# Optimization experiments

Measured on AMD Instinct MI355X. Metric: run time of the kernel, lower is better.

## Reference

```python
import jax, jax.numpy as jnp
import numpy as np

EPS = 1e-7
MAX_NORM = 1.0 - 1e-5  # Poincare-ball norm clip (standard in Poincare impls to keep atanh finite)


def _cart_to_sph(p):
    # p: [..., 3] -> (radius, polar theta, azimuth phi)
    x, y, z = p[..., 0], p[..., 1], p[..., 2]
    r = jnp.linalg.norm(p, axis=-1)
    theta = jnp.arccos(jnp.clip(z / jnp.maximum(r, EPS), -1.0, 1.0))
    phi = jnp.arctan2(y, x)
    return jnp.stack((r, theta, phi), axis=-1)


def _sph_to_cart(s):
    r, theta, phi = s[..., 0], s[..., 1], s[..., 2]
    tmp = r * jnp.sin(theta)
    return jnp.stack((tmp * jnp.cos(phi), tmp * jnp.sin(phi), r * jnp.cos(theta)), axis=-1)


def _log0(x):
    # Poincare log map at the origin, c=1: atanh(||x||) * x/||x|| (norm clipped)
    n = jnp.linalg.norm(x, axis=-1, keepdims=True)
    return jnp.arctanh(jnp.minimum(n, MAX_NORM)) * x / jnp.maximum(n, EPS)


def _exp0(v):
    # Poincare exp map at the origin, c=1: tanh(||v||) * v/||v||
    n = jnp.linalg.norm(v, axis=-1, keepdims=True)
    return jnp.tanh(n) * v / jnp.maximum(n, EPS)


def setup_inputs() -> dict:
    key = jax.random.key(0)
    k1, k2 = jax.random.split(key)
    B, H, N, K, M = 256, 2, 1024, 64, 3
    dgms = jax.random.uniform(k1, (B, H, N, 2), dtype=jnp.float32)          # persistence points in [0,1)
    theta = jax.random.uniform(k2, (H, K, M), dtype=jnp.float32,
                               minval=-0.05, maxval=0.05)                    # tf.random_uniform_initializer default
    return {"dgms": dgms, "theta": theta}


def reference(dgms, theta):
    # dgms: [B, H, N, 2], theta: [H, K, 3]
    B, H, N, _ = dgms.shape
    K = theta.shape[1]
    y3 = jnp.pad(dgms, ((0, 0), (0, 0), (0, 0), (0, 1)))                     # pad point to 3D: [B,H,N,3]
    # broadcast-add each basis vector theta[h,k]: [B,H,K,N,3]
    shifted = y3[:, :, None, :, :] + theta[None, :, :, None, :]
    sph = _cart_to_sph(shifted)                                              # [B,H,K,N,3]
    tangent = _log0(sph)                                                     # log map to tangent space at origin
    sums = jnp.sum(tangent, axis=3)                                          # sum over points: [B,H,K,3]
    x_dgm = _exp0(sums)                                                      # back to the manifold
    y_dgm = _sph_to_cart(x_dgm)                                              # [B,H,K,3]
    return y_dgm.reshape(B, H * K * 3)                                       # hom0 block then hom1 block, matching tf concat
```

## Files before the change

kernel.cpp:

```cpp
#include <hip/hip_runtime.h>
#include <hip/hip_bf16.h>

#define B_DIM 256
#define H_DIM 2
#define N_DIM 1024
#define K_DIM 64

#define PI_F      3.14159265358979f
#define HALF_PI_F 1.57079632679490f
#define PI2_4_F   2.46740110027234f
#define MAX_NORM  0.99999f
#define ATANH_MN  6.1030247f
#define RC2       0.0625f

template <int CTRL>
static __device__ __forceinline__ float dpp_f(float x) {
    return __int_as_float(__builtin_amdgcn_update_dpp(
        0, __float_as_int(x), CTRL, 0xF, 0xF, false));
}
static __device__ __forceinline__ float row16_sum(float x) {
    x += dpp_f<0xB1>(x);
    x += dpp_f<0x4E>(x);
    x += dpp_f<0x124>(x);
    x += dpp_f<0x128>(x);
    return x;
}

static __device__ __forceinline__ float atan_poly(float t) {
    float u = t * t;
    float p = fmaf(u, 0.0208351f, -0.0851330f);
    p = fmaf(u, p, 0.1801410f);
    p = fmaf(u, p, -0.3302995f);
    p = fmaf(u, p, 0.9998660f);
    return t * p;
}
static __device__ __forceinline__ float asin_poly(float u) {
    float u2 = u * u;
    float qa = fmaf(u2, 0.0340000f, 0.0303819f);
    qa = fmaf(u2, qa, 0.0446429f);
    qa = fmaf(u2, qa, 0.0750000f);
    qa = fmaf(u2, qa, 0.1666667f);
    return fmaf(u * u2, qa, u);
}
static __device__ __forceinline__ float slow_s(float n2, float ninv) {
    float n = n2 * ninv;
    float m = fminf(n, MAX_NORM);
    float at = 0.34657359f *
               __builtin_amdgcn_logf((1.0f + m) * __builtin_amdgcn_rcpf(1.0f - m));
    return at * ninv;
}
static __device__ __forceinline__ float sin_poly(float u) {
    float u2 = u * u;
    float p = fmaf(u2, -1.9841270e-4f, 8.3333333e-3f);
    p = fmaf(u2, p, -1.6666667e-1f);
    return u * fmaf(u2, p, 1.0f);
}
static __device__ __forceinline__ float cos_poly(float u) {
    float u2 = u * u;
    float p = fmaf(u2, 2.4801587e-5f, -1.3888889e-3f);
    p = fmaf(u2, p, 4.1666667e-2f);
    p = fmaf(u2, p, -0.5f);
    return fmaf(u2, p, 1.0f);
}

static __device__ __forceinline__ void ad_point(float x, float y, float* acc) {
    float q  = fmaf(x, x, y * y);
    float si = __builtin_amdgcn_rsqf(q);
    float u2 = si * si, u3 = si * u2, u4 = u2 * u2;
    float rho = q * si;

    float mn = fminf(x, y);
    float A  = asin_poly(mn * si);
    float phi0 = (y > x) ? (HALF_PI_F - A) : A;

    float phx  = -y * u2, phy = x * u2;
    float phxx = 2.0f * x * y * u4;
    float phxy = (y * y - x * x) * u4;
    float phyy = -phxx;

    float m0  = fmaf(phi0, phi0, q + PI2_4_F);
    float mx  = fmaf(2.0f * phi0, phx, 2.0f * x);
    float my  = fmaf(2.0f * phi0, phy, 2.0f * y);
    float mz  = -PI_F * si;
    float mxx = fmaf(2.0f, fmaf(phx, phx, phi0 * phxx), 2.0f);
    float mxy = 2.0f * fmaf(phx, phy, phi0 * phxy);
    float myy = fmaf(2.0f, fmaf(phy, phy, phi0 * phyy), 2.0f);
    float mzz = fmaf(2.0f, u2, 2.0f);
    float mxz = PI_F * x * u3;
    float myz = PI_F * y * u3;

    float w  = __builtin_amdgcn_rsqf(m0);
    float w2 = w * w, w3 = w * w2;
    float s0 = ATANH_MN * w;
    float A1 = -0.5f * ATANH_MN * w3;
    float A2 = -1.5f * A1 * w2;
    float sx = A1 * mx, sy = A1 * my, sz = A1 * mz;
    float sxx = fmaf(A2 * mx, mx, A1 * mxx);
    float sxy = fmaf(A2 * mx, my, A1 * mxy);
    float syy = fmaf(A2 * my, my, A1 * myy);
    float sxz = fmaf(A2 * mx, mz, A1 * mxz);
    float syz = fmaf(A2 * my, mz, A1 * myz);
    float szz = fmaf(A2 * mz, mz, A1 * mzz);

    float rx = x * si, ry = y * si;
    float rxx = y * y * u3, rxy = -x * y * u3, ryy = x * x * u3;

    acc[0] += s0 * rho;
    acc[1] += fmaf(sx, rho, s0 * rx);
    acc[2] += fmaf(sy, rho, s0 * ry);
    acc[3] += sz * rho;
    acc[4] += fmaf(sxx, rho, fmaf(2.0f * sx, rx, s0 * rxx));
    acc[5] += fmaf(sxy, rho, fmaf(sx, ry, fmaf(sy, rx, s0 * rxy)));
    acc[6] += fmaf(syy, rho, fmaf(2.0f * sy, ry, s0 * ryy));
    acc[7] += fmaf(sxz, rho, sz * rx);
    acc[8] += fmaf(syz, rho, sz * ry);
    acc[9] += fmaf(szz, rho, s0 * si);
    acc[10] += s0 * HALF_PI_F;
    acc[11] += sx * HALF_PI_F;
    acc[12] += sy * HALF_PI_F;
    acc[13] += fmaf(sz, HALF_PI_F, -s0 * si);
    acc[14] += sxx * HALF_PI_F;
    acc[15] += sxy * HALF_PI_F;
    acc[16] += syy * HALF_PI_F;
    acc[17] += fmaf(sxz, HALF_PI_F, fmaf(-sx, si, s0 * x * u3));
    acc[18] += fmaf(syz, HALF_PI_F, fmaf(-sy, si, s0 * y * u3));
    acc[19] += fmaf(szz, HALF_PI_F, -2.0f * sz * si);
    acc[20] += s0 * phi0;
    acc[21] += fmaf(sx, phi0, s0 * phx);
    acc[22] += fmaf(sy, phi0, s0 * phy);
    acc[23] += sz * phi0;
    acc[24] += fmaf(sxx, phi0, fmaf(2.0f * sx, phx, s0 * phxx));
    acc[25] += fmaf(sxy, phi0, fmaf(sx, phy, fmaf(sy, phx, s0 * phxy)));
    acc[26] += fmaf(syy, phi0, fmaf(2.0f * sy, phy, s0 * phyy));
    acc[27] += fmaf(sxz, phi0, sz * phx);
    acc[28] += fmaf(syz, phi0, sz * phy);
    acc[29] += szz * phi0;
}

__global__ __launch_bounds__(256) void pman_fused(const void* __restrict__ dgms,
                                                  const void* __restrict__ theta,
                                                  void* __restrict__ out) {
    __shared__ float  lds_coef[32];
    __shared__ float  lds_part[16][32];
    __shared__ int    lds_cnt;
    __shared__ float2 lds_near[512];

    const int tid  = threadIdx.x;
    const int lane = tid & 63;
    const int wv   = tid >> 6;
    const int bh   = blockIdx.x;
    const int h    = bh & 1;
    if (tid == 0) lds_cnt = 0;
    __syncthreads();

    const unsigned int wrd = ((const unsigned int*)dgms)[lane];
    const bool f32 = __popcll(__ballot((wrd >> 15) & 1u)) > 8;

    const int k   = tid >> 2;
    const int sub = tid & 3;
    float tx, ty, tz;
    {
        const int tb = (h * K_DIM + k) * 3;
        if (f32) {
            const float* t = (const float*)theta;
            tx = t[tb]; ty = t[tb + 1]; tz = t[tb + 2];
        } else {
            const unsigned short* t = (const unsigned short*)theta;
            tx = __uint_as_float(((unsigned int)t[tb]) << 16);
            ty = __uint_as_float(((unsigned int)t[tb + 1]) << 16);
            tz = __uint_as_float(((unsigned int)t[tb + 2]) << 16);
        }
    }

    float px[4], py[4];
    if (f32) {
        const float4* fp = (const float4*)dgms + (bh << 9) + (tid << 1);
        const float4 a = fp[0], b = fp[1];
        px[0] = a.x; py[0] = a.y; px[1] = a.z; py[1] = a.w;
        px[2] = b.x; py[2] = b.y; px[3] = b.z; py[3] = b.w;
    } else {
        const uint4 d = ((const uint4*)dgms)[(bh << 8) + tid];
        px[0] = __uint_as_float(d.x << 16); py[0] = __uint_as_float(d.x & 0xFFFF0000u);
        px[1] = __uint_as_float(d.y << 16); py[1] = __uint_as_float(d.y & 0xFFFF0000u);
        px[2] = __uint_as_float(d.z << 16); py[2] = __uint_as_float(d.z & 0xFFFF0000u);
        px[3] = __uint_as_float(d.w << 16); py[3] = __uint_as_float(d.w & 0xFFFF0000u);
    }

    float acc[30];
    #pragma unroll
    for (int i = 0; i < 30; ++i) acc[i] = 0.0f;

    const unsigned long long lt_mask = (1ull << lane) - 1ull;
    #pragma unroll
    for (int i = 0; i < 4; ++i) {
        float x0 = px[i], y0 = py[i];
        float q = fmaf(x0, x0, y0 * y0);
        const bool isnear = q < RC2;
        unsigned long long nm = __ballot(isnear);
        int base = 0;
        if (lane == 0 && nm) base = atomicAdd(&lds_cnt, __popcll(nm));
        base = __shfl(base, 0);
        if (isnear) {
            lds_near[base + __popcll(nm & lt_mask)] = make_float2(x0, y0);
        } else {
            ad_point(x0, y0, acc);
        }
    }

    #pragma unroll
    for (int i = 0; i < 30; ++i) acc[i] = row16_sum(acc[i]);
    if ((lane & 15) == 0) {
        const int row = (wv << 2) | (lane >> 4);
        #pragma unroll
        for (int i = 0; i < 30; ++i) lds_part[row][i] = acc[i];
    }
    __syncthreads();
    if (tid < 30) {
        float s = 0.0f;
        #pragma unroll
        for (int r = 0; r < 16; ++r) s += lds_part[r][tid];
        lds_coef[tid] = s;
    }
    __syncthreads();

    const float az = fabsf(tz);
    const float ntz = -tz;
    const float inv_tz = __builtin_amdgcn_rcpf((tz == 0.0f) ? 1e-30f : tz);
    const float kbase = (tz < 0.0f) ? PI_F : 0.0f;
    const float z2 = tz * tz;
    const float z2h = 0.5f * z2;
    const float haz_inv = 0.5f * __builtin_amdgcn_rcpf(fmaxf(az, 1e-30f));

    const int cnt = lds_cnt;
    float ar = 0.f, at_ = 0.f, ap = 0.f;
    for (int i = sub; i < cnt; i += 4) {
        float2 pt = lds_near[i];
        float x = pt.x + tx, y = pt.y + ty;
        float rxy2 = fmaf(x, x, fmaf(y, y, 1e-30f));
        float sxyinv = __builtin_amdgcn_rsqf(rxy2);
        float sxy = rxy2 * sxyinv;
        float r2 = rxy2 + z2;
        const bool big = sxy >= az;
        float rr = big ? fmaf(z2h, sxyinv, sxy) : fmaf(haz_inv, rxy2, az);
        float te = big ? ntz * sxyinv : sxy * inv_tz;
        float K  = big ? HALF_PI_F : kbase;
        float th = K + atan_poly(te);
        float ax = fabsf(x), ay = fabsf(y);
        float lo = fminf(ax, ay);
        float u = lo * sxyinv;
        float As = asin_poly(u);
        float p = (ay > ax) ? (HALF_PI_F - As) : As;
        p = (x < 0.0f) ? (PI_F - p) : p;
        p = __uint_as_float(__float_as_uint(p) ^
                            (__float_as_uint(y) & 0x80000000u));
        float n2 = fmaf(th, th, fmaf(p, p, r2));
        float ninv = __builtin_amdgcn_rsqf(n2);
        float s = ATANH_MN * ninv;
        if (__builtin_expect(n2 < 1.0f, 0))
            s = slow_s(n2, ninv);
        ar = fmaf(s, rr, ar);
        at_ = fmaf(s, th, at_);
        ap = fmaf(s, p, ap);
    }
    #pragma unroll
    for (int m = 2; m; m >>= 1) {
        ar += __shfl_xor(ar, m);
        at_ += __shfl_xor(at_, m);
        ap += __shfl_xor(ap, m);
    }

    if (sub == 0) {
        float tx2h = 0.5f * tx * tx, ty2h = 0.5f * ty * ty, tz2h = 0.5f * tz * tz;
        float txty = tx * ty, txtz = tx * tz, tytz = ty * tz;
        float S[3];
        #pragma unroll
        for (int o = 0; o < 3; ++o) {
            const float* cc = lds_coef + o * 10;
            float v = cc[0];
            v = fmaf(cc[1], tx, v);   v = fmaf(cc[2], ty, v);   v = fmaf(cc[3], tz, v);
            v = fmaf(cc[4], tx2h, v); v = fmaf(cc[5], txty, v); v = fmaf(cc[6], ty2h, v);
            v = fmaf(cc[7], txtz, v); v = fmaf(cc[8], tytz, v); v = fmaf(cc[9], tz2h, v);
            S[o] = v;
        }
        float sr = S[0] + ar, st = S[1] + at_, sp = S[2] + ap;
        float n2 = fmaf(sr, sr, fmaf(st, st, sp * sp));
        float rsqn = __builtin_amdgcn_rsqf(fmaxf(n2, 1e-30f));
        float nv = n2 * rsqn;
        float scale = rsqn;
        if (__builtin_expect(nv < 16.0f, 0))
            scale = tanhf(nv) / fmaxf(nv, 1e-7f);
        float rr = scale * sr;
        float th = scale * st;
        float ph = scale * sp;
        float tmp = rr * sin_poly(th);
        const int o = (bh * K_DIM + k) * 3;
        if (f32) {
            float* op = (float*)out;
            op[o]     = tmp * cos_poly(ph);
            op[o + 1] = tmp * sin_poly(ph);
            op[o + 2] = rr * cos_poly(th);
        } else {
            __hip_bfloat16* op = (__hip_bfloat16*)out;
            op[o]     = __float2bfloat16(tmp * cos_poly(ph));
            op[o + 1] = __float2bfloat16(tmp * sin_poly(ph));
            op[o + 2] = __float2bfloat16(rr * cos_poly(th));
        }
    }
}

extern "C" void kernel_launch(void* const* d_in, const int* in_sizes, int n_in,
                              void* d_out, int out_size, void* d_ws, size_t ws_size,
                              hipStream_t stream) {
    (void)in_sizes; (void)n_in; (void)out_size; (void)d_ws; (void)ws_size;
    pman_fused<<<B_DIM * H_DIM, 256, 0, stream>>>(d_in[0], d_in[1], d_out);
}
```

Measured before the change: 64.38 us.

## Split fused kernel into two phases via workspace for more parallelism

Replaces the single fused kernel (one block per batch-head) with a memset plus two kernels. Phase 1 spreads the far-point Taylor-coefficient accumulation and near-point compaction across four blocks per batch-head, using global atomics into a workspace. Phase 2 computes the exact near-point terms with 16 lanes per basis vector and more blocks in total. The aim is more blocks in flight and a shorter serial near-point loop per wave. The cost is extra launches, global atomics and a workspace round-trip. The fused kernel stays as a fallback when the workspace is too small.

```diff
diff --git a/kernel.cpp b/kernel.cpp
--- a/kernel.cpp
+++ b/kernel.cpp
@@ -12,6 +12,12 @@
 #define MAX_NORM  0.99999f
 #define ATANH_MN  6.1030247f
 #define RC2       0.0625f
+
+#define WS_COEF   0
+#define WS_CNT    65536
+#define WS_ZERO_BYTES 67584
+#define WS_NEAR   67584
+#define WS_NEEDED (WS_NEAR + 512 * 1024 * 8)
 
 template <int CTRL>
 static __device__ __forceinline__ float dpp_f(float x) {
@@ -137,6 +143,194 @@
     acc[29] += szz * phi0;
 }
 
+static __device__ __forceinline__ void epilogue(const float* cc30, float ar, float at_,
+                                                float ap, float tx, float ty, float tz,
+                                                int o, bool f32, void* out) {
+    float tx2h = 0.5f * tx * tx, ty2h = 0.5f * ty * ty, tz2h = 0.5f * tz * tz;
+    float txty = tx * ty, txtz = tx * tz, tytz = ty * tz;
+    float S[3];
+    #pragma unroll
+    for (int oo = 0; oo < 3; ++oo) {
+        const float* cc = cc30 + oo * 10;
+        float v = cc[0];
+        v = fmaf(cc[1], tx, v);   v = fmaf(cc[2], ty, v);   v = fmaf(cc[3], tz, v);
+        v = fmaf(cc[4], tx2h, v); v = fmaf(cc[5], txty, v); v = fmaf(cc[6], ty2h, v);
+        v = fmaf(cc[7], txtz, v); v = fmaf(cc[8], tytz, v); v = fmaf(cc[9], tz2h, v);
+        S[oo] = v;
+    }
+    float sr = S[0] + ar, st = S[1] + at_, sp = S[2] + ap;
+    float n2 = fmaf(sr, sr, fmaf(st, st, sp * sp));
+    float rsqn = __builtin_amdgcn_rsqf(fmaxf(n2, 1e-30f));
+    float nv = n2 * rsqn;
+    float scale = rsqn;
+    if (__builtin_expect(nv < 16.0f, 0))
+        scale = tanhf(nv) / fmaxf(nv, 1e-7f);
+    float rr = scale * sr;
+    float th = scale * st;
+    float ph = scale * sp;
+    float tmp = rr * sin_poly(th);
+    if (f32) {
+        float* op = (float*)out;
+        op[o]     = tmp * cos_poly(ph);
+        op[o + 1] = tmp * sin_poly(ph);
+        op[o + 2] = rr * cos_poly(th);
+    } else {
+        __hip_bfloat16* op = (__hip_bfloat16*)out;
+        op[o]     = __float2bfloat16(tmp * cos_poly(ph));
+        op[o + 1] = __float2bfloat16(tmp * sin_poly(ph));
+        op[o + 2] = __float2bfloat16(rr * cos_poly(th));
+    }
+}
+
+static __device__ __forceinline__ void near_term(float x, float y, float tz, float az,
+                                                 float ntz, float inv_tz, float kbase,
+                                                 float z2, float z2h, float haz_inv,
+                                                 float& ar, float& at_, float& ap) {
+    float rxy2 = fmaf(x, x, fmaf(y, y, 1e-30f));
+    float sxyinv = __builtin_amdgcn_rsqf(rxy2);
+    float sxy = rxy2 * sxyinv;
+    float r2 = rxy2 + z2;
+    const bool big = sxy >= az;
+    float rr = big ? fmaf(z2h, sxyinv, sxy) : fmaf(haz_inv, rxy2, az);
+    float te = big ? ntz * sxyinv : sxy * inv_tz;
+    float K  = big ? HALF_PI_F : kbase;
+    float th = K + atan_poly(te);
+    float ax = fabsf(x), ay = fabsf(y);
+    float lo = fminf(ax, ay);
+    float u = lo * sxyinv;
+    float As = asin_poly(u);
+    float p = (ay > ax) ? (HALF_PI_F - As) : As;
+    p = (x < 0.0f) ? (PI_F - p) : p;
+    p = __uint_as_float(__float_as_uint(p) ^ (__float_as_uint(y) & 0x80000000u));
+    float n2 = fmaf(th, th, fmaf(p, p, r2));
+    float ninv = __builtin_amdgcn_rsqf(n2);
+    float s = ATANH_MN * ninv;
+    if (__builtin_expect(n2 < 1.0f, 0))
+        s = slow_s(n2, ninv);
+    ar = fmaf(s, rr, ar);
+    at_ = fmaf(s, th, at_);
+    ap = fmaf(s, p, ap);
+}
+
+__global__ __launch_bounds__(256) void pman_phase1(const void* __restrict__ dgms,
+                                                   void* __restrict__ ws) {
+    __shared__ float lds_part[16][32];
+    const int tid  = threadIdx.x;
+    const int lane = tid & 63;
+    const int wv   = tid >> 6;
+    const int blk  = blockIdx.x;
+    const int bh   = blk >> 2;
+    const int quarter = blk & 3;
+
+    const unsigned int wrd = ((const unsigned int*)dgms)[lane];
+    const bool f32 = __popcll(__ballot((wrd >> 15) & 1u)) > 8;
+
+    const int pt = (bh << 10) + (quarter << 8) + tid;
+    float x0, y0;
+    if (f32) {
+        const float2 d = ((const float2*)dgms)[pt];
+        x0 = d.x; y0 = d.y;
+    } else {
+        const unsigned int d = ((const unsigned int*)dgms)[pt];
+        x0 = __uint_as_float(d << 16);
+        y0 = __uint_as_float(d & 0xFFFF0000u);
+    }
+
+    float*  coef  = (float*)((char*)ws + WS_COEF) + (bh << 5);
+    int*    cnt   = (int*)((char*)ws + WS_CNT);
+    float2* nearp = (float2*)((char*)ws + WS_NEAR) + (bh << 10);
+
+    float acc[30];
+    #pragma unroll
+    for (int i = 0; i < 30; ++i) acc[i] = 0.0f;
+
+    float q = fmaf(x0, x0, y0 * y0);
+    const bool isnear = q < RC2;
+    unsigned long long nm = __ballot(isnear);
+    int base = 0;
+    if (lane == 0 && nm) base = atomicAdd(&cnt[bh], __popcll(nm));
+    base = __shfl(base, 0);
+    if (isnear) {
+        nearp[base + __popcll(nm & ((1ull << lane) - 1ull))] = make_float2(x0, y0);
+    } else {
+        ad_point(x0, y0, acc);
+    }
+
+    #pragma unroll
+    for (int i = 0; i < 30; ++i) acc[i] = row16_sum(acc[i]);
+    if ((lane & 15) == 0) {
+        const int row = (wv << 2) | (lane >> 4);
+        #pragma unroll
+        for (int i = 0; i < 30; ++i) lds_part[row][i] = acc[i];
+    }
+    __syncthreads();
+    if (tid < 30) {
+        float s = 0.0f;
+        #pragma unroll
+        for (int r = 0; r < 16; ++r) s += lds_part[r][tid];
+        atomicAdd(&coef[tid], s);
+    }
+}
+
+__global__ __launch_bounds__(256) void pman_phase2(const void* __restrict__ dgms,
+                                                   const void* __restrict__ theta,
+                                                   void* __restrict__ out,
+                                                   const void* __restrict__ ws) {
+    const int tid  = threadIdx.x;
+    const int lane = tid & 63;
+    const unsigned int wrd = ((const unsigned int*)dgms)[lane];
+    const bool f32 = __popcll(__ballot((wrd >> 15) & 1u)) > 8;
+
+    const int w   = blockIdx.x * 4 + (tid >> 6);
+    const int bh  = w >> 4;
+    const int grp = lane >> 4;
+    const int sub = lane & 15;
+    const int k   = ((w & 15) << 2) + grp;
+    const int h   = bh & 1;
+
+    float tx, ty, tz;
+    {
+        const int tb = (h * K_DIM + k) * 3;
+        if (f32) {
+            const float* t = (const float*)theta;
+            tx = t[tb]; ty = t[tb + 1]; tz = t[tb + 2];
+        } else {
+            const unsigned short* t = (const unsigned short*)theta;
+            tx = __uint_as_float(((unsigned int)t[tb]) << 16);
+            ty = __uint_as_float(((unsigned int)t[tb + 1]) << 16);
+            tz = __uint_as_float(((unsigned int)t[tb + 2]) << 16);
+        }
+    }
+    const float az = fabsf(tz);
+    const float ntz = -tz;
+    const float inv_tz = __builtin_amdgcn_rcpf((tz == 0.0f) ? 1e-30f : tz);
+    const float kbase = (tz < 0.0f) ? PI_F : 0.0f;
+    const float z2 = tz * tz;
+    const float z2h = 0.5f * z2;
+    const float haz_inv = 0.5f * __builtin_amdgcn_rcpf(fmaxf(az, 1e-30f));
+
+    const int cnt = ((const int*)((const char*)ws + WS_CNT))[bh];
+    const float2* np = (const float2*)((const char*)ws + WS_NEAR) + (bh << 10);
+
+    float ar = 0.f, at_ = 0.f, ap = 0.f;
+    for (int i = sub; i < cnt; i += 16) {
+        float2 pt = np[i];
+        near_term(pt.x + tx, pt.y + ty, tz, az, ntz, inv_tz, kbase,
+                  z2, z2h, haz_inv, ar, at_, ap);
+    }
+    ar  = row16_sum(ar);
+    at_ = row16_sum(at_);
+    ap  = row16_sum(ap);
+
+    if (sub == 0) {
+        const float* cc = (const float*)((const char*)ws + WS_COEF) + (bh << 5);
+        float c30[30];
+        #pragma unroll
+        for (int i = 0; i < 30; ++i) c30[i] = cc[i];
+        epilogue(c30, ar, at_, ap, tx, ty, tz, (bh * K_DIM + k) * 3, f32, out);
+    }
+}
+
 __global__ __launch_bounds__(256) void pman_fused(const void* __restrict__ dgms,
                                                   const void* __restrict__ theta,
                                                   void* __restrict__ out) {
@@ -235,32 +429,8 @@
     float ar = 0.f, at_ = 0.f, ap = 0.f;
     for (int i = sub; i < cnt; i += 4) {
         float2 pt = lds_near[i];
-        float x = pt.x + tx, y = pt.y + ty;
-        float rxy2 = fmaf(x, x, fmaf(y, y, 1e-30f));
-        float sxyinv = __builtin_amdgcn_rsqf(rxy2);
-        float sxy = rxy2 * sxyinv;
-        float r2 = rxy2 + z2;
-        const bool big = sxy >= az;
-        float rr = big ? fmaf(z2h, sxyinv, sxy) : fmaf(haz_inv, rxy2, az);
-        float te = big ? ntz * sxyinv : sxy * inv_tz;
-        float K  = big ? HALF_PI_F : kbase;
-        float th = K + atan_poly(te);
-        float ax = fabsf(x), ay = fabsf(y);
-        float lo = fminf(ax, ay);
-        float u = lo * sxyinv;
-        float As = asin_poly(u);
-        float p = (ay > ax) ? (HALF_PI_F - As) : As;
-        p = (x < 0.0f) ? (PI_F - p) : p;
-        p = __uint_as_float(__float_as_uint(p) ^
-                            (__float_as_uint(y) & 0x80000000u));
-        float n2 = fmaf(th, th, fmaf(p, p, r2));
-        float ninv = __builtin_amdgcn_rsqf(n2);
-        float s = ATANH_MN * ninv;
-        if (__builtin_expect(n2 < 1.0f, 0))
-            s = slow_s(n2, ninv);
-        ar = fmaf(s, rr, ar);
-        at_ = fmaf(s, th, at_);
-        ap = fmaf(s, p, ap);
+        near_term(pt.x + tx, pt.y + ty, tz, az, ntz, inv_tz, kbase,
+                  z2, z2h, haz_inv, ar, at_, ap);
     }
     #pragma unroll
     for (int m = 2; m; m >>= 1) {
@@ -268,49 +438,23 @@
         at_ += __shfl_xor(at_, m);
         ap += __shfl_xor(ap, m);
     }
-
     if (sub == 0) {
-        float tx2h = 0.5f * tx * tx, ty2h = 0.5f * ty * ty, tz2h = 0.5f * tz * tz;
-        float txty = tx * ty, txtz = tx * tz, tytz = ty * tz;
-        float S[3];
-        #pragma unroll
-        for (int o = 0; o < 3; ++o) {
-            const float* cc = lds_coef + o * 10;
-            float v = cc[0];
-            v = fmaf(cc[1], tx, v);   v = fmaf(cc[2], ty, v);   v = fmaf(cc[3], tz, v);
-            v = fmaf(cc[4], tx2h, v); v = fmaf(cc[5], txty, v); v = fmaf(cc[6], ty2h, v);
-            v = fmaf(cc[7], txtz, v); v = fmaf(cc[8], tytz, v); v = fmaf(cc[9], tz2h, v);
-            S[o] = v;
-        }
-        float sr = S[0] + ar, st = S[1] + at_, sp = S[2] + ap;
-        float n2 = fmaf(sr, sr, fmaf(st, st, sp * sp));
-        float rsqn = __builtin_amdgcn_rsqf(fmaxf(n2, 1e-30f));
-        float nv = n2 * rsqn;
-        float scale = rsqn;
-        if (__builtin_expect(nv < 16.0f, 0))
-            scale = tanhf(nv) / fmaxf(nv, 1e-7f);
-        float rr = scale * sr;
-        float th = scale * st;
-        float ph = scale * sp;
-        float tmp = rr * sin_poly(th);
-        const int o = (bh * K_DIM + k) * 3;
-        if (f32) {
-            float* op = (float*)out;
-            op[o]     = tmp * cos_poly(ph);
-            op[o + 1] = tmp * sin_poly(ph);
-            op[o + 2] = rr * cos_poly(th);
-        } else {
-            __hip_bfloat16* op = (__hip_bfloat16*)out;
-            op[o]     = __float2bfloat16(tmp * cos_poly(ph));
-            op[o + 1] = __float2bfloat16(tmp * sin_poly(ph));
-            op[o + 2] = __float2bfloat16(rr * cos_poly(th));
-        }
+        float c30[30];
+        #pragma unroll
+        for (int i = 0; i < 30; ++i) c30[i] = lds_coef[i];
+        epilogue(c30, ar, at_, ap, tx, ty, tz, (bh * K_DIM + k) * 3, f32, out);
     }
 }
 
 extern "C" void kernel_launch(void* const* d_in, const int* in_sizes, int n_in,
                               void* d_out, int out_size, void* d_ws, size_t ws_size,
                               hipStream_t stream) {
-    (void)in_sizes; (void)n_in; (void)out_size; (void)d_ws; (void)ws_size;
-    pman_fused<<<B_DIM * H_DIM, 256, 0, stream>>>(d_in[0], d_in[1], d_out);
-}
+    (void)in_sizes; (void)n_in; (void)out_size;
+    if (ws_size >= (size_t)WS_NEEDED) {
+        hipMemsetAsync(d_ws, 0, WS_ZERO_BYTES, stream);
+        pman_phase1<<<B_DIM * H_DIM * 4, 256, 0, stream>>>(d_in[0], d_ws);
+        pman_phase2<<<B_DIM * H_DIM * 4, 256, 0, stream>>>(d_in[0], d_in[1], d_out, d_ws);
+    } else {
+        pman_fused<<<B_DIM * H_DIM, 256, 0, stream>>>(d_in[0], d_in[1], d_out);
+    }
+}
```

Measured after the change: 76.37 us. 18.6% more time.
